# Kernel tuning notes

Hardware: AMD Instinct MI355X
Metric: run time of the kernel (lower is better)

The kernel has to match this reference:

```python
import jax, jax.numpy as jnp
import numpy as np

B, M, N_CTR, K = 16, 2048, 512, 32
DIM, DEPTH, HEADS = 384, 6, 6
EMB = 48  # fourier embedding dim (48//6 = 8 freqs per axis, basis [3,24])


def make_basis():
    e = (2.0 ** np.arange(EMB // 6)).astype(np.float32) * np.pi  # [8]
    z = np.zeros(EMB // 6, np.float32)
    basis = np.stack([np.concatenate([e, z, z]),
                      np.concatenate([z, e, z]),
                      np.concatenate([z, z, e])])  # [3, 24]
    return jnp.asarray(basis)


def fourier_embed(x, basis):
    # x [..., 3] -> [..., 48]  (sin/cos of 24 frequency projections)
    p = jnp.einsum('...d,de->...e', x, basis)
    return jnp.concatenate([jnp.sin(p), jnp.cos(p)], axis=-1)


def fps_idx(pos, n):
    # farthest point sampling, deterministic start at index 0. pos [M,3] -> [n]
    d0 = jnp.sum((pos - pos[0]) ** 2, -1)
    def step(d, _):
        i = jnp.argmax(d)
        d = jnp.minimum(d, jnp.sum((pos - pos[i]) ** 2, -1))
        return d, i
    _, idxs = jax.lax.scan(step, d0, None, length=n - 1)
    return jnp.concatenate([jnp.zeros(1, jnp.int32), idxs.astype(jnp.int32)])


def layernorm(x, g, b, eps=1e-6):
    m = jnp.mean(x, -1, keepdims=True)
    v = jnp.var(x, -1, keepdims=True)
    return (x - m) * jax.lax.rsqrt(v + eps) * g + b


def _lin(key, fi, fo):
    kw, kb = jax.random.split(key)
    w = jax.random.normal(kw, (fi, fo), jnp.float32) / np.sqrt(fi)
    b = jax.random.normal(kb, (fo,), jnp.float32) * 0.01
    return w, b


def setup_inputs() -> dict:
    key = jax.random.key(0)
    ks = jax.random.split(key, 16)
    pc = jax.random.uniform(ks[0], (B, M, 3), jnp.float32)
    embed_w, embed_b = _lin(ks[1], 3 + EMB, DIM)
    lw1, lb1 = _lin(ks[2], 3 + EMB, 256)
    lw2, lb2 = _lin(ks[3], 256, 256)
    gw1, gb1 = _lin(ks[4], 256, 256)
    gw2, gb2 = _lin(ks[5], 256, DIM)
    def stack_lin(k, fi, fo):
        kk = jax.random.split(k, DEPTH)
        ws, bs = zip(*[_lin(kk[i], fi, fo) for i in range(DEPTH)])
        return jnp.stack(ws), jnp.stack(bs)
    qkv_w, qkv_b = stack_lin(ks[6], DIM, 3 * DIM)
    proj_w, proj_b = stack_lin(ks[7], DIM, DIM)
    fc1_w, fc1_b = stack_lin(ks[8], DIM, 4 * DIM)
    fc2_w, fc2_b = stack_lin(ks[9], 4 * DIM, DIM)
    return dict(
        pc=pc, embed_w=embed_w, embed_b=embed_b,
        lw1=lw1, lb1=lb1, lw2=lw2, lb2=lb2,
        gw1=gw1, gb1=gb1, gw2=gw2, gb2=gb2,
        ln1_g=jnp.ones((DEPTH, DIM)), ln1_b=jnp.zeros((DEPTH, DIM)),
        qkv_w=qkv_w, qkv_b=qkv_b, proj_w=proj_w, proj_b=proj_b,
        gamma1=jax.random.normal(ks[10], (DEPTH, DIM)) * 0.1,
        ln2_g=jnp.ones((DEPTH, DIM)), ln2_b=jnp.zeros((DEPTH, DIM)),
        fc1_w=fc1_w, fc1_b=fc1_b, fc2_w=fc2_w, fc2_b=fc2_b,
        gamma2=jax.random.normal(ks[11], (DEPTH, DIM)) * 0.1,
        lnf_g=jnp.ones((DIM,)), lnf_b=jnp.zeros((DIM,)),
    )


def reference(pc, embed_w, embed_b, lw1, lb1, lw2, lb2, gw1, gb1, gw2, gb2,
              ln1_g, ln1_b, qkv_w, qkv_b, proj_w, proj_b, gamma1,
              ln2_g, ln2_b, fc1_w, fc1_b, fc2_w, fc2_b, gamma2, lnf_g, lnf_b):
    basis = make_basis()
    # --- FPS centers (per batch) ---
    idx = jax.vmap(lambda p: fps_idx(p, N_CTR))(pc)                 # [B,N]
    centers = jnp.take_along_axis(pc, idx[:, :, None], axis=1)      # [B,N,3]
    # --- KNN graph: for each center, K nearest of the M points ---
    d2 = jnp.sum((centers[:, :, None, :] - pc[:, None, :, :]) ** 2, -1)  # [B,N,M]
    _, nn_idx = jax.lax.top_k(-d2, K)                               # [B,N,K]
    # --- PointConv: gather -> local MLP -> max-scatter -> global MLP ---
    src = jax.vmap(lambda p, i: p[i])(pc, nn_idx)                   # [B,N,K,3]
    rel = src - centers[:, :, None, :]
    feat = jnp.concatenate([rel, fourier_embed(rel, basis)], -1)    # [B,N,K,51]
    h = jax.nn.relu(feat @ lw1 + lb1) @ lw2 + lb2                   # [B,N,K,256]
    h = jnp.max(h, axis=2)  # scatter_max over edges == max over K neighbors
    x = jax.nn.relu(h @ gw1 + gb1) @ gw2 + gb2                      # [B,N,DIM]
    # --- positional embedding tokens ---
    pe = jnp.concatenate([centers, fourier_embed(centers, basis)], -1) @ embed_w + embed_b
    x = x + pe
    # --- ViT blocks (pre-LN, LayerScale, eval mode: no dropout/droppath) ---
    hd = DIM // HEADS
    scale = hd ** -0.5
    for l in range(DEPTH):
        xn = layernorm(x, ln1_g[l], ln1_b[l])
        qkv = (xn @ qkv_w[l] + qkv_b[l]).reshape(B, N_CTR, 3, HEADS, hd)
        q, k, v = jnp.moveaxis(qkv, 2, 0)                           # [B,N,H,hd]
        att = jax.nn.softmax(jnp.einsum('bqhd,bkhd->bhqk', q, k) * scale, axis=-1)
        o = jnp.einsum('bhqk,bkhd->bqhd', att, v).reshape(B, N_CTR, DIM)
        x = x + gamma1[l] * (o @ proj_w[l] + proj_b[l])
        xn = layernorm(x, ln2_g[l], ln2_b[l])
        mlp = jax.nn.gelu(xn @ fc1_w[l] + fc1_b[l], approximate=False) @ fc2_w[l] + fc2_b[l]
        x = x + gamma2[l] * mlp
    out = layernorm(x, lnf_g, lnf_b)
    return out, centers
```

## Files before the change

kernel.cpp:

```cpp
#include <hip/hip_runtime.h>
#include <math.h>

#define NB 16
#define NM 2048
#define NCTR 512
#define NK 32
#define NDIM 384

typedef unsigned long long ull;
typedef unsigned int uint;
typedef unsigned short ushort;
typedef __attribute__((ext_vector_type(8))) short bf16x8;
typedef __attribute__((ext_vector_type(4))) float f32x4;

__device__ __forceinline__ float dist2_exact(float ax, float ay, float az,
                                             float bx, float by, float bz) {
  float dx = __fsub_rn(ax, bx);
  float dy = __fsub_rn(ay, by);
  float dz = __fsub_rn(az, bz);
  return __fadd_rn(__fadd_rn(__fmul_rn(dx, dx), __fmul_rn(dy, dy)),
                   __fmul_rn(dz, dz));
}

__device__ __forceinline__ float gelu_f(float x) {
  return 0.5f * x * (1.0f + erff(x * 0.70710678118654752f));
}

__device__ __forceinline__ ushort f2bf(float f) {
  uint u = __float_as_uint(f);
  return (ushort)((u + 0x7FFFu + ((u >> 16) & 1u)) >> 16);
}
__device__ __forceinline__ float bf2f(ushort h) {
  return __uint_as_float(((uint)h) << 16);
}

__device__ __forceinline__ void cvt8(float4 p, float4 q, uint4& hi, uint4& lo) {
  float v0 = p.x, v1 = p.y, v2 = p.z, v3 = p.w;
  float v4 = q.x, v5 = q.y, v6 = q.z, v7 = q.w;
  ushort h0 = f2bf(v0), h1 = f2bf(v1), h2 = f2bf(v2), h3 = f2bf(v3);
  ushort h4 = f2bf(v4), h5 = f2bf(v5), h6 = f2bf(v6), h7 = f2bf(v7);
  ushort l0 = f2bf(v0 - bf2f(h0)), l1 = f2bf(v1 - bf2f(h1));
  ushort l2 = f2bf(v2 - bf2f(h2)), l3 = f2bf(v3 - bf2f(h3));
  ushort l4 = f2bf(v4 - bf2f(h4)), l5 = f2bf(v5 - bf2f(h5));
  ushort l6 = f2bf(v6 - bf2f(h6)), l7 = f2bf(v7 - bf2f(h7));
  hi.x = (uint)h0 | ((uint)h1 << 16); hi.y = (uint)h2 | ((uint)h3 << 16);
  hi.z = (uint)h4 | ((uint)h5 << 16); hi.w = (uint)h6 | ((uint)h7 << 16);
  lo.x = (uint)l0 | ((uint)l1 << 16); lo.y = (uint)l2 | ((uint)l3 << 16);
  lo.z = (uint)l4 | ((uint)l5 << 16); lo.w = (uint)l6 | ((uint)l7 << 16);
}

__global__ __launch_bounds__(256)
void fps_kernel(const float* __restrict__ pc, float* __restrict__ centers) {
  int b = blockIdx.x;
  __shared__ float4 pos4[NM];
  __shared__ ull red[2][4];
  const float* pb = pc + (size_t)b * (NM * 3);
  int tid = threadIdx.x, lane = tid & 63, wv = tid >> 6;
  float px[8], py[8], pz[8];
#pragma unroll
  for (int i = 0; i < 8; ++i) {
    int p = tid + 256 * i;
    float x = pb[3 * p], y = pb[3 * p + 1], z = pb[3 * p + 2];
    px[i] = x; py[i] = y; pz[i] = z;
    pos4[p] = make_float4(x, y, z, 0.f);
  }
  __syncthreads();
  float* cb = centers + (size_t)b * (NCTR * 3);
  float4 s0 = pos4[0];
  float sx = s0.x, sy = s0.y, sz = s0.z;
  if (tid == 0) { cb[0] = sx; cb[1] = sy; cb[2] = sz; }
  float d[8];
  for (int n = 1; n < NCTR; ++n) {
    ull best = 0;
#pragma unroll
    for (int i = 0; i < 8; ++i) {
      int p = tid + 256 * i;
      float nd = dist2_exact(px[i], py[i], pz[i], sx, sy, sz);
      d[i] = (n == 1) ? nd : fminf(d[i], nd);
      ull key = ((ull)__float_as_uint(d[i]) << 32) | (unsigned)(0x7FFFFFFF - p);
      best = best > key ? best : key;
    }
#pragma unroll
    for (int off = 32; off; off >>= 1) {
      ull o = __shfl_xor(best, off);
      best = best > o ? best : o;
    }
    if (lane == 0) red[n & 1][wv] = best;
    __syncthreads();
    ull g0 = red[n & 1][0], g1 = red[n & 1][1];
    ull g2 = red[n & 1][2], g3 = red[n & 1][3];
    ull ga = g0 > g1 ? g0 : g1;
    ull gc2 = g2 > g3 ? g2 : g3;
    ull gb = ga > gc2 ? ga : gc2;
    int j = 0x7FFFFFFF - (int)(unsigned)(gb & 0xFFFFFFFFull);
    float4 np = pos4[j];
    sx = np.x; sy = np.y; sz = np.z;
    if (tid == 0) { cb[n * 3] = sx; cb[n * 3 + 1] = sy; cb[n * 3 + 2] = sz; }
  }
}

__global__ __launch_bounds__(256, 2)
void knn_kernel(const float* __restrict__ pc, const float* __restrict__ centers,
                int* __restrict__ nn) {
  __shared__ float pos[NM * 3];
  int b = blockIdx.x >> 7;
  int n0 = (blockIdx.x & 127) << 2;
  const float* pb = pc + (size_t)b * (NM * 3);
  for (int i = threadIdx.x; i < NM * 3; i += 256) pos[i] = pb[i];
  __syncthreads();
  int wv = threadIdx.x >> 6, lane = threadIdx.x & 63;
  int gc = b * NCTR + n0 + wv;
  float cx = centers[gc * 3], cy = centers[gc * 3 + 1], cz = centers[gc * 3 + 2];
  ull key[32];
  ull gmin[4];
#pragma unroll
  for (int g = 0; g < 4; ++g) {
    gmin[g] = ~0ull;
#pragma unroll
    for (int i = 0; i < 8; ++i) {
      int r = g * 8 + i;
      int p = lane + (r << 6);
      float nd = dist2_exact(pos[3 * p], pos[3 * p + 1], pos[3 * p + 2], cx, cy, cz);
      key[r] = ((ull)__float_as_uint(nd) << 11) | (unsigned)p;
      gmin[g] = gmin[g] < key[r] ? gmin[g] : key[r];
    }
  }
  ull a01 = gmin[0] < gmin[1] ? gmin[0] : gmin[1];
  ull a23 = gmin[2] < gmin[3] ? gmin[2] : gmin[3];
  ull lmin = a01 < a23 ? a01 : a23;
  int* nnc = nn + (size_t)gc * NK;
  for (int round = 0; round < NK; ++round) {
    ull w = lmin;
#pragma unroll
    for (int off = 32; off; off >>= 1) {
      ull o = __shfl_xor(w, off);
      w = w < o ? w : o;
    }
    if (lmin == w) {
      nnc[round] = (int)(w & 2047ull);
#pragma unroll
      for (int g = 0; g < 4; ++g) {
        if (gmin[g] == w) {
          gmin[g] = ~0ull;
#pragma unroll
          for (int i = 0; i < 8; ++i) {
            int r = g * 8 + i;
            key[r] = (key[r] == w) ? ~0ull : key[r];
            gmin[g] = gmin[g] < key[r] ? gmin[g] : key[r];
          }
        }
      }
      ull b01 = gmin[0] < gmin[1] ? gmin[0] : gmin[1];
      ull b23 = gmin[2] < gmin[3] ? gmin[2] : gmin[3];
      lmin = b01 < b23 ? b01 : b23;
    }
  }
}

__global__ __launch_bounds__(256)
void wconv(const float* __restrict__ W, ushort* __restrict__ out, int K8, int N,
           int Ksrc) {
  int c = blockIdx.x * 256 + threadIdx.x;
  if (c >= K8 * N) return;
  int kb = c / N, n = c - kb * N;
  float v[8];
#pragma unroll
  for (int i = 0; i < 8; ++i) {
    int row = kb * 8 + i;
    v[i] = (row < Ksrc) ? W[(size_t)row * N + n] : 0.f;
  }
  float4 p, q;
  p.x = v[0]; p.y = v[1]; p.z = v[2]; p.w = v[3];
  q.x = v[4]; q.y = v[5]; q.z = v[6]; q.w = v[7];
  uint4 hi, lo;
  cvt8(p, q, hi, lo);
  *(uint4*)(out + (size_t)c * 8) = hi;
  *(uint4*)(out + (size_t)(K8 * N + c) * 8) = lo;
}

__global__ __launch_bounds__(256, 2)
void edge_mfma(const float* __restrict__ pc, const float* __restrict__ centers,
               const int* __restrict__ nn, const ushort* __restrict__ lw1s,
               const float* __restrict__ lb1, const ushort* __restrict__ lw2s,
               const float* __restrict__ lb2, float* __restrict__ h) {
  __shared__ __align__(16) ushort featH[4096], featL[4096];
  __shared__ __align__(16) ushort t1H[16384], t1L[16384];
  int tid = threadIdx.x;
  int w = tid >> 6, lane = tid & 63;
  int l15 = lane & 15, l4 = lane >> 4;
  int wbase = w << 6;
  {
    int e = tid >> 2, s = tid & 3;
    int ge = blockIdx.x * 64 + e;
    int c = ge >> 5;
    int b = c >> 9;
    int j = nn[ge];
    const float* sp = pc + ((size_t)b * NM + j) * 3;
    float rx = sp[0] - centers[c * 3];
    float ry = sp[1] - centers[c * 3 + 1];
    float rz = sp[2] - centers[c * 3 + 2];
    auto putk = [&](int k, float v) {
      ushort hi = f2bf(v);
      ushort lo = f2bf(v - bf2f(hi));
      int idx = ((k >> 3) * 64 + e) * 8 + (k & 7);
      featH[idx] = hi;
      featL[idx] = lo;
    };
    if (s < 3) {
      float r = (s == 0) ? rx : (s == 1) ? ry : rz;
#pragma unroll
      for (int f = 0; f < 8; ++f) {
        float ef = (float)(M_PI * (double)(1 << f));
        float p = r * ef;
        putk(3 + 8 * s + f, sinf(p));
        putk(27 + 8 * s + f, cosf(p));
      }
    } else {
      putk(0, rx);
      putk(1, ry);
      putk(2, rz);
#pragma unroll
      for (int k = 51; k < 64; ++k) putk(k, 0.f);
    }
  }
  __syncthreads();
  const ushort* lw1H = lw1s;
  const ushort* lw1L = lw1s + 8 * 256 * 8;
  f32x4 acc1[4][4];
#pragma unroll
  for (int i = 0; i < 4; ++i)
#pragma unroll
    for (int j = 0; j < 4; ++j) acc1[i][j] = (f32x4){0.f, 0.f, 0.f, 0.f};
#pragma unroll
  for (int ks = 0; ks < 2; ++ks) {
    bf16x8 ah[4], al[4];
#pragma unroll
    for (int fm = 0; fm < 4; ++fm) {
      int idx = ((ks * 4 + l4) * 64 + fm * 16 + l15) * 8;
      ah[fm] = *(const bf16x8*)&featH[idx];
      al[fm] = *(const bf16x8*)&featL[idx];
    }
#pragma unroll
    for (int fn = 0; fn < 4; ++fn) {
      int col = wbase + fn * 16 + l15;
      size_t boff = ((size_t)(ks * 4 + l4) * 256 + col) * 8;
      bf16x8 bh = *(const bf16x8*)(lw1H + boff);
      bf16x8 bl = *(const bf16x8*)(lw1L + boff);
#pragma unroll
      for (int fm = 0; fm < 4; ++fm) {
        acc1[fm][fn] = __builtin_amdgcn_mfma_f32_16x16x32_bf16(al[fm], bh, acc1[fm][fn], 0, 0, 0);
        acc1[fm][fn] = __builtin_amdgcn_mfma_f32_16x16x32_bf16(ah[fm], bl, acc1[fm][fn], 0, 0, 0);
        acc1[fm][fn] = __builtin_amdgcn_mfma_f32_16x16x32_bf16(ah[fm], bh, acc1[fm][fn], 0, 0, 0);
      }
    }
  }
#pragma unroll
  for (int fn = 0; fn < 4; ++fn) {
    int chan = wbase + fn * 16 + l15;
    float bias = lb1[chan];
    int kb = chan >> 3, k7 = chan & 7;
#pragma unroll
    for (int fm = 0; fm < 4; ++fm) {
#pragma unroll
      for (int r = 0; r < 4; ++r) {
        int edge = fm * 16 + l4 * 4 + r;
        float v = fmaxf(acc1[fm][fn][r] + bias, 0.f);
        ushort hi = f2bf(v);
        ushort lo = f2bf(v - bf2f(hi));
        int idx = (kb * 64 + edge) * 8 + k7;
        t1H[idx] = hi;
        t1L[idx] = lo;
      }
    }
  }
  __syncthreads();
  const ushort* lw2H = lw2s;
  const ushort* lw2L = lw2s + 32 * 256 * 8;
  f32x4 acc2[4][4];
#pragma unroll
  for (int i = 0; i < 4; ++i)
#pragma unroll
    for (int j = 0; j < 4; ++j) acc2[i][j] = (f32x4){0.f, 0.f, 0.f, 0.f};
#pragma unroll
  for (int ks = 0; ks < 8; ++ks) {
    bf16x8 ah[4], al[4];
#pragma unroll
    for (int fm = 0; fm < 4; ++fm) {
      int idx = ((ks * 4 + l4) * 64 + fm * 16 + l15) * 8;
      ah[fm] = *(const bf16x8*)&t1H[idx];
      al[fm] = *(const bf16x8*)&t1L[idx];
    }
#pragma unroll
    for (int fn = 0; fn < 4; ++fn) {
      int col = wbase + fn * 16 + l15;
      size_t boff = ((size_t)(ks * 4 + l4) * 256 + col) * 8;
      bf16x8 bh = *(const bf16x8*)(lw2H + boff);
      bf16x8 bl = *(const bf16x8*)(lw2L + boff);
#pragma unroll
      for (int fm = 0; fm < 4; ++fm) {
        acc2[fm][fn] = __builtin_amdgcn_mfma_f32_16x16x32_bf16(al[fm], bh, acc2[fm][fn], 0, 0, 0);
        acc2[fm][fn] = __builtin_amdgcn_mfma_f32_16x16x32_bf16(ah[fm], bl, acc2[fm][fn], 0, 0, 0);
        acc2[fm][fn] = __builtin_amdgcn_mfma_f32_16x16x32_bf16(ah[fm], bh, acc2[fm][fn], 0, 0, 0);
      }
    }
  }
#pragma unroll
  for (int fn = 0; fn < 4; ++fn) {
    int col = wbase + fn * 16 + l15;
    float m0 = -INFINITY, m1 = -INFINITY;
#pragma unroll
    for (int r = 0; r < 4; ++r) {
      m0 = fmaxf(m0, fmaxf(acc2[0][fn][r], acc2[1][fn][r]));
      m1 = fmaxf(m1, fmaxf(acc2[2][fn][r], acc2[3][fn][r]));
    }
    m0 = fmaxf(m0, __shfl_xor(m0, 16));
    m0 = fmaxf(m0, __shfl_xor(m0, 32));
    m1 = fmaxf(m1, __shfl_xor(m1, 16));
    m1 = fmaxf(m1, __shfl_xor(m1, 32));
    if (l4 == 0) {
      float bias = lb2[col];
      int c0 = blockIdx.x * 2;
      h[(size_t)c0 * 256 + col] = m0 + bias;
      h[(size_t)(c0 + 1) * 256 + col] = m1 + bias;
    }
  }
}

template <int EPI>
__global__ __launch_bounds__(256, 2)
void gemm_x3(const float* __restrict__ A, const ushort* __restrict__ Wh,
             const ushort* __restrict__ Wl, const float* __restrict__ bias,
             const float* __restrict__ gamma, const float* __restrict__ resid,
             float* __restrict__ C, int M, int N, int K) {
  __shared__ __align__(16) ushort Ah[4096], Al[4096], Bh[4096], Bl[4096];
  int tid = threadIdx.x;
  int bn = blockIdx.x << 7, bm = blockIdx.y << 7;
  int wid = tid >> 6, lane = tid & 63;
  int wr = wid >> 1, wc = wid & 1;
  int l15 = lane & 15, l4 = lane >> 4;

  int arow = tid >> 1, akb0 = (tid & 1) << 1;
  const float* Ap = A + (size_t)(bm + arow) * K + (akb0 << 3);
  int wkb = tid >> 7, wn = tid & 127;

  f32x4 acc[4][4];
#pragma unroll
  for (int i = 0; i < 4; ++i)
#pragma unroll
    for (int j = 0; j < 4; ++j) acc[i][j] = (f32x4){0.f, 0.f, 0.f, 0.f};

  float4 a0 = *(const float4*)(Ap + 0);
  float4 a1 = *(const float4*)(Ap + 4);
  float4 a2 = *(const float4*)(Ap + 8);
  float4 a3 = *(const float4*)(Ap + 12);
  size_t wo1 = ((size_t)wkb * N + bn + wn) * 8;
  size_t wo2 = ((size_t)(wkb + 2) * N + bn + wn) * 8;
  uint4 w0 = *(const uint4*)(Wh + wo1);
  uint4 w1 = *(const uint4*)(Wh + wo2);
  uint4 w2 = *(const uint4*)(Wl + wo1);
  uint4 w3 = *(const uint4*)(Wl + wo2);

  int nkt = K >> 5;
  for (int kt = 0; kt < nkt; ++kt) {
    uint4 h0, l0, h1, l1;
    cvt8(a0, a1, h0, l0);
    cvt8(a2, a3, h1, l1);
    *(uint4*)&Ah[(akb0 * 128 + arow) * 8] = h0;
    *(uint4*)&Ah[((akb0 + 1) * 128 + arow) * 8] = h1;
    *(uint4*)&Al[(akb0 * 128 + arow) * 8] = l0;
    *(uint4*)&Al[((akb0 + 1) * 128 + arow) * 8] = l1;
    *(uint4*)&Bh[tid * 8] = w0;
    *(uint4*)&Bh[(tid + 256) * 8] = w1;
    *(uint4*)&Bl[tid * 8] = w2;
    *(uint4*)&Bl[(tid + 256) * 8] = w3;
    __syncthreads();
    if (kt + 1 < nkt) {
      const float* Apn = Ap + ((kt + 1) << 5);
      a0 = *(const float4*)(Apn + 0);
      a1 = *(const float4*)(Apn + 4);
      a2 = *(const float4*)(Apn + 8);
      a3 = *(const float4*)(Apn + 12);
      size_t b1 = ((size_t)((kt + 1) * 4 + wkb) * N + bn + wn) * 8;
      size_t b2 = ((size_t)((kt + 1) * 4 + wkb + 2) * N + bn + wn) * 8;
      w0 = *(const uint4*)(Wh + b1);
      w1 = *(const uint4*)(Wh + b2);
      w2 = *(const uint4*)(Wl + b1);
      w3 = *(const uint4*)(Wl + b2);
    }
    bf16x8 ahf[4], alf[4];
#pragma unroll
    for (int fm = 0; fm < 4; ++fm) {
      int ci = l4 * 128 + wr * 64 + fm * 16 + l15;
      ahf[fm] = *(bf16x8*)&Ah[ci * 8];
      alf[fm] = *(bf16x8*)&Al[ci * 8];
    }
#pragma unroll
    for (int fn = 0; fn < 4; ++fn) {
      int ci = l4 * 128 + wc * 64 + fn * 16 + l15;
      bf16x8 bh = *(bf16x8*)&Bh[ci * 8];
      bf16x8 bl = *(bf16x8*)&Bl[ci * 8];
#pragma unroll
      for (int fm = 0; fm < 4; ++fm) {
        acc[fm][fn] = __builtin_amdgcn_mfma_f32_16x16x32_bf16(alf[fm], bh, acc[fm][fn], 0, 0, 0);
        acc[fm][fn] = __builtin_amdgcn_mfma_f32_16x16x32_bf16(ahf[fm], bl, acc[fm][fn], 0, 0, 0);
        acc[fm][fn] = __builtin_amdgcn_mfma_f32_16x16x32_bf16(ahf[fm], bh, acc[fm][fn], 0, 0, 0);
      }
    }
    __syncthreads();
  }

#pragma unroll
  for (int fn = 0; fn < 4; ++fn) {
    int col = bn + wc * 64 + fn * 16 + l15;
    float bv = bias[col];
    float gv = (EPI == 3) ? gamma[col] : 0.f;
#pragma unroll
    for (int fm = 0; fm < 4; ++fm) {
      int row0 = bm + wr * 64 + fm * 16 + l4 * 4;
#pragma unroll
      for (int r = 0; r < 4; ++r) {
        float v = acc[fm][fn][r] + bv;
        if (EPI == 1) v = fmaxf(v, 0.f);
        else if (EPI == 2) v = gelu_f(v);
        else if (EPI == 3) v = resid[(size_t)(row0 + r) * N + col] + gv * v;
        C[(size_t)(row0 + r) * N + col] = v;
      }
    }
  }
}

__global__ __launch_bounds__(256)
void pe_add(const float* __restrict__ centers, const float* __restrict__ ew,
            const float* __restrict__ eb, float* x) {
  __shared__ float fc[51];
  int c = blockIdx.x, tid = threadIdx.x;
  if (tid < 24) {
    int a = tid >> 3, f = tid & 7;
    float coord = centers[c * 3 + a];
    float p = coord * (float)(M_PI * (double)(1 << f));
    fc[3 + tid] = sinf(p);
    fc[27 + tid] = cosf(p);
  } else if (tid < 27) {
    fc[tid - 24] = centers[c * 3 + (tid - 24)];
  }
  __syncthreads();
  for (int j = tid; j < NDIM; j += 256) {
    float acc = eb[j];
#pragma unroll
    for (int d = 0; d < 51; ++d) acc = fmaf(fc[d], ew[d * NDIM + j], acc);
    x[(size_t)c * NDIM + j] += acc;
  }
}

__global__ __launch_bounds__(256)
void ln_f32(const float* __restrict__ x, const float* __restrict__ g,
            const float* __restrict__ b, float* __restrict__ y) {
  int row = (blockIdx.x << 2) + (threadIdx.x >> 6);
  int lane = threadIdx.x & 63;
  const float* xr = x + (size_t)row * NDIM;
  float v[6];
#pragma unroll
  for (int i = 0; i < 6; ++i) v[i] = xr[lane + (i << 6)];
  float s = 0.f;
#pragma unroll
  for (int i = 0; i < 6; ++i) s += v[i];
#pragma unroll
  for (int off = 32; off; off >>= 1) s += __shfl_xor(s, off);
  float m = s / 384.f;
  float var = 0.f;
#pragma unroll
  for (int i = 0; i < 6; ++i) { float dd = v[i] - m; var += dd * dd; }
#pragma unroll
  for (int off = 32; off; off >>= 1) var += __shfl_xor(var, off);
  var = var / 384.f;
  float rs = 1.f / sqrtf(var + 1e-6f);
#pragma unroll
  for (int i = 0; i < 6; ++i) {
    int cc = lane + (i << 6);
    y[(size_t)row * NDIM + cc] = (v[i] - m) * rs * g[cc] + b[cc];
  }
}

__global__ __launch_bounds__(256, 2)
void attn_mfma(const float* __restrict__ qkv, float* __restrict__ o) {
  __shared__ __align__(16) ushort kTH[4096], kTL[4096];
  __shared__ __align__(16) ushort vSH[4096], vSL[4096];
  __shared__ __align__(16) ushort pSH[8192], pSL[8192];
  int bi = blockIdx.x;
  int qt = bi & 3;
  int hh = (bi >> 2) % 6;
  int b = bi / 24;
  int tid = threadIdx.x;
  int w = tid >> 6, lane = tid & 63;
  int l15 = lane & 15, l4 = lane >> 4;
  const float* base = qkv + (size_t)(b * NCTR) * 1152;
  int qbase = qt * 128 + w * 32;

  bf16x8 qh[2][2], ql[2][2];
#pragma unroll
  for (int qr = 0; qr < 2; ++qr) {
#pragma unroll
    for (int ds = 0; ds < 2; ++ds) {
      const float* qp = base + (size_t)(qbase + qr * 16 + l15) * 1152 + hh * 64 +
                        ds * 32 + l4 * 8;
      float4 f0 = *(const float4*)qp;
      float4 f1 = *(const float4*)(qp + 4);
      uint4 hi, lo;
      cvt8(f0, f1, hi, lo);
      qh[qr][ds] = *(bf16x8*)&hi;
      ql[qr][ds] = *(bf16x8*)&lo;
    }
  }

  f32x4 oacc[2][4];
#pragma unroll
  for (int i = 0; i < 2; ++i)
#pragma unroll
    for (int j = 0; j < 4; ++j) oacc[i][j] = (f32x4){0.f, 0.f, 0.f, 0.f};
  float m_[2][4], l_[2][4];
#pragma unroll
  for (int i = 0; i < 2; ++i)
#pragma unroll
    for (int r = 0; r < 4; ++r) { m_[i][r] = -INFINITY; l_[i][r] = 0.f; }

  ushort* pHw = pSH + w * 2048;
  ushort* pLw = pSL + w * 2048;

  for (int ch = 0; ch < 8; ++ch) {
    {
      int key = tid & 63, dgh = tid >> 6;
      const float* kp = base + (size_t)(ch * 64 + key) * 1152 + 384 + hh * 64;
#pragma unroll
      for (int i = 0; i < 2; ++i) {
        int dg = dgh * 2 + i;
        float4 f0 = *(const float4*)(kp + dg * 8);
        float4 f1 = *(const float4*)(kp + dg * 8 + 4);
        uint4 hi, lo;
        cvt8(f0, f1, hi, lo);
        *(uint4*)&kTH[(dg * 64 + key) * 8] = hi;
        *(uint4*)&kTL[(dg * 64 + key) * 8] = lo;
      }
      int d = tid & 63, kb2 = tid >> 6;
#pragma unroll
      for (int i = 0; i < 2; ++i) {
        int kb = kb2 + i * 4;
        float vv[8];
#pragma unroll
        for (int j = 0; j < 8; ++j)
          vv[j] = base[(size_t)(ch * 64 + kb * 8 + j) * 1152 + 768 + hh * 64 + d];
        float4 f0, f1;
        f0.x = vv[0]; f0.y = vv[1]; f0.z = vv[2]; f0.w = vv[3];
        f1.x = vv[4]; f1.y = vv[5]; f1.z = vv[6]; f1.w = vv[7];
        uint4 hi, lo;
        cvt8(f0, f1, hi, lo);
        *(uint4*)&vSH[(kb * 64 + d) * 8] = hi;
        *(uint4*)&vSL[(kb * 64 + d) * 8] = lo;
      }
    }
    __syncthreads();

    f32x4 sacc[2][4];
#pragma unroll
    for (int i = 0; i < 2; ++i)
#pragma unroll
      for (int j = 0; j < 4; ++j) sacc[i][j] = (f32x4){0.f, 0.f, 0.f, 0.f};
#pragma unroll
    for (int ds = 0; ds < 2; ++ds) {
#pragma unroll
      for (int kc = 0; kc < 4; ++kc) {
        int idx = ((ds * 4 + l4) * 64 + kc * 16 + l15) * 8;
        bf16x8 bh = *(const bf16x8*)&kTH[idx];
        bf16x8 bl = *(const bf16x8*)&kTL[idx];
#pragma unroll
        for (int qr = 0; qr < 2; ++qr) {
          sacc[qr][kc] = __builtin_amdgcn_mfma_f32_16x16x32_bf16(ql[qr][ds], bh, sacc[qr][kc], 0, 0, 0);
          sacc[qr][kc] = __builtin_amdgcn_mfma_f32_16x16x32_bf16(qh[qr][ds], bl, sacc[qr][kc], 0, 0, 0);
          sacc[qr][kc] = __builtin_amdgcn_mfma_f32_16x16x32_bf16(qh[qr][ds], bh, sacc[qr][kc], 0, 0, 0);
        }
      }
    }

    float t[2][4];
#pragma unroll
    for (int qr = 0; qr < 2; ++qr)
#pragma unroll
      for (int r = 0; r < 4; ++r) {
        float a0 = sacc[qr][0][r] * 0.125f; sacc[qr][0][r] = a0;
        float a1 = sacc[qr][1][r] * 0.125f; sacc[qr][1][r] = a1;
        float a2 = sacc[qr][2][r] * 0.125f; sacc[qr][2][r] = a2;
        float a3 = sacc[qr][3][r] * 0.125f; sacc[qr][3][r] = a3;
        t[qr][r] = fmaxf(fmaxf(a0, a1), fmaxf(a2, a3));
      }
#pragma unroll
    for (int off = 1; off < 16; off <<= 1)
#pragma unroll
      for (int qr = 0; qr < 2; ++qr)
#pragma unroll
        for (int r = 0; r < 4; ++r)
          t[qr][r] = fmaxf(t[qr][r], __shfl_xor(t[qr][r], off));
    float f_[2][4];
#pragma unroll
    for (int qr = 0; qr < 2; ++qr)
#pragma unroll
      for (int r = 0; r < 4; ++r) {
        float mn = fmaxf(m_[qr][r], t[qr][r]);
        f_[qr][r] = expf(m_[qr][r] - mn);
        m_[qr][r] = mn;
      }
#pragma unroll
    for (int qr = 0; qr < 2; ++qr)
#pragma unroll
      for (int dc = 0; dc < 4; ++dc)
#pragma unroll
        for (int r = 0; r < 4; ++r) oacc[qr][dc][r] *= f_[qr][r];
    float sm[2][4];
#pragma unroll
    for (int qr = 0; qr < 2; ++qr)
#pragma unroll
      for (int r = 0; r < 4; ++r) {
        float p0 = expf(sacc[qr][0][r] - m_[qr][r]); sacc[qr][0][r] = p0;
        float p1 = expf(sacc[qr][1][r] - m_[qr][r]); sacc[qr][1][r] = p1;
        float p2 = expf(sacc[qr][2][r] - m_[qr][r]); sacc[qr][2][r] = p2;
        float p3 = expf(sacc[qr][3][r] - m_[qr][r]); sacc[qr][3][r] = p3;
        sm[qr][r] = ((p0 + p1) + (p2 + p3));
      }
#pragma unroll
    for (int off = 1; off < 16; off <<= 1)
#pragma unroll
      for (int qr = 0; qr < 2; ++qr)
#pragma unroll
        for (int r = 0; r < 4; ++r)
          sm[qr][r] += __shfl_xor(sm[qr][r], off);
#pragma unroll
    for (int qr = 0; qr < 2; ++qr)
#pragma unroll
      for (int r = 0; r < 4; ++r) l_[qr][r] = l_[qr][r] * f_[qr][r] + sm[qr][r];

#pragma unroll
    for (int qr = 0; qr < 2; ++qr)
#pragma unroll
      for (int kc = 0; kc < 4; ++kc)
#pragma unroll
        for (int r = 0; r < 4; ++r) {
          float pv = sacc[qr][kc][r];
          ushort hi = f2bf(pv);
          ushort lo = f2bf(pv - bf2f(hi));
          int k = kc * 16 + l15;
          int qrow = qr * 16 + l4 * 4 + r;
          int idx = ((k >> 3) * 32 + qrow) * 8 + (k & 7);
          pHw[idx] = hi;
          pLw[idx] = lo;
        }

#pragma unroll
    for (int ks = 0; ks < 2; ++ks) {
      bf16x8 pah[2], pal[2];
#pragma unroll
      for (int qr = 0; qr < 2; ++qr) {
        int idx = ((ks * 4 + l4) * 32 + qr * 16 + l15) * 8;
        pah[qr] = *(const bf16x8*)&pHw[idx];
        pal[qr] = *(const bf16x8*)&pLw[idx];
      }
#pragma unroll
      for (int dc = 0; dc < 4; ++dc) {
        int idx = ((ks * 4 + l4) * 64 + dc * 16 + l15) * 8;
        bf16x8 vh = *(const bf16x8*)&vSH[idx];
        bf16x8 vl = *(const bf16x8*)&vSL[idx];
#pragma unroll
        for (int qr = 0; qr < 2; ++qr) {
          oacc[qr][dc] = __builtin_amdgcn_mfma_f32_16x16x32_bf16(pal[qr], vh, oacc[qr][dc], 0, 0, 0);
          oacc[qr][dc] = __builtin_amdgcn_mfma_f32_16x16x32_bf16(pah[qr], vl, oacc[qr][dc], 0, 0, 0);
          oacc[qr][dc] = __builtin_amdgcn_mfma_f32_16x16x32_bf16(pah[qr], vh, oacc[qr][dc], 0, 0, 0);
        }
      }
    }
    __syncthreads();
  }

  float il[2][4];
#pragma unroll
  for (int qr = 0; qr < 2; ++qr)
#pragma unroll
    for (int r = 0; r < 4; ++r) il[qr][r] = 1.f / l_[qr][r];
#pragma unroll
  for (int qr = 0; qr < 2; ++qr)
#pragma unroll
    for (int dc = 0; dc < 4; ++dc)
#pragma unroll
      for (int r = 0; r < 4; ++r) {
        int row = b * NCTR + qbase + qr * 16 + l4 * 4 + r;
        int col = hh * 64 + dc * 16 + l15;
        o[(size_t)row * NDIM + col] = oacc[qr][dc][r] * il[qr][r];
      }
}

extern "C" void kernel_launch(void* const* d_in, const int* in_sizes, int n_in,
                              void* d_out, int out_size, void* d_ws, size_t ws_size,
                              hipStream_t stream) {
  const float* pc      = (const float*)d_in[0];
  const float* embed_w = (const float*)d_in[1];
  const float* embed_b = (const float*)d_in[2];
  const float* lw1     = (const float*)d_in[3];
  const float* lb1     = (const float*)d_in[4];
  const float* lw2     = (const float*)d_in[5];
  const float* lb2     = (const float*)d_in[6];
  const float* gw1     = (const float*)d_in[7];
  const float* gb1     = (const float*)d_in[8];
  const float* gw2     = (const float*)d_in[9];
  const float* gb2     = (const float*)d_in[10];
  const float* ln1_g   = (const float*)d_in[11];
  const float* ln1_b   = (const float*)d_in[12];
  const float* qkv_w   = (const float*)d_in[13];
  const float* qkv_b   = (const float*)d_in[14];
  const float* proj_w  = (const float*)d_in[15];
  const float* proj_b  = (const float*)d_in[16];
  const float* gamma1  = (const float*)d_in[17];
  const float* ln2_g   = (const float*)d_in[18];
  const float* ln2_b   = (const float*)d_in[19];
  const float* fc1_w   = (const float*)d_in[20];
  const float* fc1_b   = (const float*)d_in[21];
  const float* fc2_w   = (const float*)d_in[22];
  const float* fc2_b   = (const float*)d_in[23];
  const float* gamma2  = (const float*)d_in[24];
  const float* lnf_g   = (const float*)d_in[25];
  const float* lnf_b   = (const float*)d_in[26];

  float* out = (float*)d_out;
  float* centers = out + (size_t)NB * NCTR * NDIM;

  int* nn = (int*)d_ws;
  float* fws = (float*)d_ws;
  float* h  = fws + 262144;
  float* x  = h + 8192 * 256;
  float* xn = x + 8192 * 384;
  float* F  = xn + 8192 * 384;
  ushort* wsplit = (ushort*)(fws + 21233664);

  size_t wofs = 0;
  ushort* qkvH[6]; ushort* projH[6]; ushort* fc1H[6]; ushort* fc2H[6];
  auto convp = [&](const float* w, int Kpad, int N, int Ksrc) -> ushort* {
    ushort* dst = wsplit + wofs;
    int K8 = Kpad >> 3, total = K8 * N;
    wconv<<<(total + 255) / 256, 256, 0, stream>>>(w, dst, K8, N, Ksrc);
    wofs += (size_t)2 * Kpad * N;
    return dst;
  };
  for (int l = 0; l < 6; ++l) qkvH[l] = convp(qkv_w + (size_t)l * 384 * 1152, 384, 1152, 384);
  for (int l = 0; l < 6; ++l) projH[l] = convp(proj_w + (size_t)l * 384 * 384, 384, 384, 384);
  for (int l = 0; l < 6; ++l) fc1H[l] = convp(fc1_w + (size_t)l * 384 * 1536, 384, 1536, 384);
  for (int l = 0; l < 6; ++l) fc2H[l] = convp(fc2_w + (size_t)l * 1536 * 384, 1536, 384, 1536);
  ushort* g1H = convp(gw1, 256, 256, 256);
  ushort* g2H = convp(gw2, 256, 384, 256);
  ushort* lw1s = convp(lw1, 64, 256, 51);
  ushort* lw2s = convp(lw2, 256, 256, 256);

  fps_kernel<<<NB, 256, 0, stream>>>(pc, centers);
  knn_kernel<<<2048, 256, 0, stream>>>(pc, centers, nn);
  edge_mfma<<<4096, 256, 0, stream>>>(pc, centers, nn, lw1s, lb1, lw2s, lb2, h);

  gemm_x3<1><<<dim3(2, 64), 256, 0, stream>>>(h, g1H, g1H + 256 * 256, gb1,
                                              nullptr, nullptr, xn, 8192, 256, 256);
  gemm_x3<0><<<dim3(3, 64), 256, 0, stream>>>(xn, g2H, g2H + 256 * 384, gb2,
                                              nullptr, nullptr, x, 8192, 384, 256);
  pe_add<<<8192, 256, 0, stream>>>(centers, embed_w, embed_b, x);

  for (int l = 0; l < 6; ++l) {
    ln_f32<<<2048, 256, 0, stream>>>(x, ln1_g + l * 384, ln1_b + l * 384, xn);
    gemm_x3<0><<<dim3(9, 64), 256, 0, stream>>>(
        xn, qkvH[l], qkvH[l] + 384 * 1152, qkv_b + l * 1152, nullptr, nullptr, F,
        8192, 1152, 384);
    attn_mfma<<<384, 256, 0, stream>>>(F, xn);
    gemm_x3<3><<<dim3(3, 64), 256, 0, stream>>>(
        xn, projH[l], projH[l] + 384 * 384, proj_b + l * 384, gamma1 + l * 384, x, x,
        8192, 384, 384);
    ln_f32<<<2048, 256, 0, stream>>>(x, ln2_g + l * 384, ln2_b + l * 384, xn);
    gemm_x3<2><<<dim3(12, 64), 256, 0, stream>>>(
        xn, fc1H[l], fc1H[l] + 384 * 1536, fc1_b + l * 1536, nullptr, nullptr, F,
        8192, 1536, 384);
    gemm_x3<3><<<dim3(3, 64), 256, 0, stream>>>(
        F, fc2H[l], fc2H[l] + 1536 * 384, fc2_b + l * 384, gamma2 + l * 384, x, x,
        8192, 384, 1536);
  }
  ln_f32<<<2048, 256, 0, stream>>>(x, lnf_g, lnf_b, out);
}
```

Measured before the change: 2.073 ms.

## Store activations pre-split as bf16 hi/lo pairs to skip per-tile conversion

Producers (edge kernel, GEMM epilogues, layernorm, attention output) now write activations as bf16 hi/lo ushort pairs instead of fp32. GEMM and attention load these directly into LDS, which removes the repeated fp32-to-bf16x2 split on every tile load, and reuse across column blocks no longer repeats that work. Memory traffic stays about the same (two ushorts per float), but conversion ALU work is removed from the GEMM inner loop. Stacked per-layer weights are also converted in one launch per tensor rather than six. The workspace layout is reorganized to hold the split buffers.

```diff
diff --git a/kernel.cpp b/kernel.cpp
--- a/kernel.cpp
+++ b/kernel.cpp
@@ -47,6 +47,13 @@
   hi.z = (uint)h4 | ((uint)h5 << 16); hi.w = (uint)h6 | ((uint)h7 << 16);
   lo.x = (uint)l0 | ((uint)l1 << 16); lo.y = (uint)l2 | ((uint)l3 << 16);
   lo.z = (uint)l4 | ((uint)l5 << 16); lo.w = (uint)l6 | ((uint)l7 << 16);
+}
+
+__device__ __forceinline__ void split_store(float v, ushort* H, ushort* L,
+                                            size_t off) {
+  ushort hi = f2bf(v);
+  H[off] = hi;
+  L[off] = f2bf(v - bf2f(hi));
 }
 
 __global__ __launch_bounds__(256)
@@ -182,7 +189,8 @@
 void edge_mfma(const float* __restrict__ pc, const float* __restrict__ centers,
                const int* __restrict__ nn, const ushort* __restrict__ lw1s,
                const float* __restrict__ lb1, const ushort* __restrict__ lw2s,
-               const float* __restrict__ lb2, float* __restrict__ h) {
+               const float* __restrict__ lb2, ushort* __restrict__ hH,
+               ushort* __restrict__ hL) {
   __shared__ __align__(16) ushort featH[4096], featL[4096];
   __shared__ __align__(16) ushort t1H[16384], t1L[16384];
   int tid = threadIdx.x;
@@ -320,18 +328,20 @@
     if (l4 == 0) {
       float bias = lb2[col];
       int c0 = blockIdx.x * 2;
-      h[(size_t)c0 * 256 + col] = m0 + bias;
-      h[(size_t)(c0 + 1) * 256 + col] = m1 + bias;
-    }
-  }
-}
-
-template <int EPI>
+      split_store(m0 + bias, hH, hL, (size_t)c0 * 256 + col);
+      split_store(m1 + bias, hH, hL, (size_t)(c0 + 1) * 256 + col);
+    }
+  }
+}
+
+template <int EPI, int OUTS>
 __global__ __launch_bounds__(256, 2)
-void gemm_x3(const float* __restrict__ A, const ushort* __restrict__ Wh,
-             const ushort* __restrict__ Wl, const float* __restrict__ bias,
-             const float* __restrict__ gamma, const float* __restrict__ resid,
-             float* __restrict__ C, int M, int N, int K) {
+void gemm_s(const ushort* __restrict__ AH, const ushort* __restrict__ AL,
+            const ushort* __restrict__ Wh, const ushort* __restrict__ Wl,
+            const float* __restrict__ bias, const float* __restrict__ gamma,
+            const float* __restrict__ resid, float* __restrict__ C,
+            ushort* __restrict__ CH, ushort* __restrict__ CL,
+            int M, int N, int K) {
   __shared__ __align__(16) ushort Ah[4096], Al[4096], Bh[4096], Bl[4096];
   int tid = threadIdx.x;
   int bn = blockIdx.x << 7, bm = blockIdx.y << 7;
@@ -340,7 +350,8 @@
   int l15 = lane & 15, l4 = lane >> 4;
 
   int arow = tid >> 1, akb0 = (tid & 1) << 1;
-  const float* Ap = A + (size_t)(bm + arow) * K + (akb0 << 3);
+  const ushort* ApH = AH + (size_t)(bm + arow) * K + (akb0 << 3);
+  const ushort* ApL = AL + (size_t)(bm + arow) * K + (akb0 << 3);
   int wkb = tid >> 7, wn = tid & 127;
 
   f32x4 acc[4][4];
@@ -349,10 +360,10 @@
 #pragma unroll
     for (int j = 0; j < 4; ++j) acc[i][j] = (f32x4){0.f, 0.f, 0.f, 0.f};
 
-  float4 a0 = *(const float4*)(Ap + 0);
-  float4 a1 = *(const float4*)(Ap + 4);
-  float4 a2 = *(const float4*)(Ap + 8);
-  float4 a3 = *(const float4*)(Ap + 12);
+  uint4 a0 = *(const uint4*)(ApH + 0);
+  uint4 a1 = *(const uint4*)(ApH + 8);
+  uint4 a2 = *(const uint4*)(ApL + 0);
+  uint4 a3 = *(const uint4*)(ApL + 8);
   size_t wo1 = ((size_t)wkb * N + bn + wn) * 8;
   size_t wo2 = ((size_t)(wkb + 2) * N + bn + wn) * 8;
   uint4 w0 = *(const uint4*)(Wh + wo1);
@@ -362,24 +373,20 @@
 
   int nkt = K >> 5;
   for (int kt = 0; kt < nkt; ++kt) {
-    uint4 h0, l0, h1, l1;
-    cvt8(a0, a1, h0, l0);
-    cvt8(a2, a3, h1, l1);
-    *(uint4*)&Ah[(akb0 * 128 + arow) * 8] = h0;
-    *(uint4*)&Ah[((akb0 + 1) * 128 + arow) * 8] = h1;
-    *(uint4*)&Al[(akb0 * 128 + arow) * 8] = l0;
-    *(uint4*)&Al[((akb0 + 1) * 128 + arow) * 8] = l1;
+    *(uint4*)&Ah[(akb0 * 128 + arow) * 8] = a0;
+    *(uint4*)&Ah[((akb0 + 1) * 128 + arow) * 8] = a1;
+    *(uint4*)&Al[(akb0 * 128 + arow) * 8] = a2;
+    *(uint4*)&Al[((akb0 + 1) * 128 + arow) * 8] = a3;
     *(uint4*)&Bh[tid * 8] = w0;
     *(uint4*)&Bh[(tid + 256) * 8] = w1;
     *(uint4*)&Bl[tid * 8] = w2;
     *(uint4*)&Bl[(tid + 256) * 8] = w3;
     __syncthreads();
     if (kt + 1 < nkt) {
-      const float* Apn = Ap + ((kt + 1) << 5);
-      a0 = *(const float4*)(Apn + 0);
-      a1 = *(const float4*)(Apn + 4);
-      a2 = *(const float4*)(Apn + 8);
-      a3 = *(const float4*)(Apn + 12);
+      a0 = *(const uint4*)(ApH + (kt + 1) * 32 + 0);
+      a1 = *(const uint4*)(ApH + (kt + 1) * 32 + 8);
+      a2 = *(const uint4*)(ApL + (kt + 1) * 32 + 0);
+      a3 = *(const uint4*)(ApL + (kt + 1) * 32 + 8);
       size_t b1 = ((size_t)((kt + 1) * 4 + wkb) * N + bn + wn) * 8;
       size_t b2 = ((size_t)((kt + 1) * 4 + wkb + 2) * N + bn + wn) * 8;
       w0 = *(const uint4*)(Wh + b1);
@@ -423,7 +430,9 @@
         if (EPI == 1) v = fmaxf(v, 0.f);
         else if (EPI == 2) v = gelu_f(v);
         else if (EPI == 3) v = resid[(size_t)(row0 + r) * N + col] + gv * v;
-        C[(size_t)(row0 + r) * N + col] = v;
+        size_t off = (size_t)(row0 + r) * N + col;
+        if (OUTS == 0) C[off] = v;
+        else split_store(v, CH, CL, off);
       }
     }
   }
@@ -481,8 +490,40 @@
   }
 }
 
+__global__ __launch_bounds__(256)
+void ln_split(const float* __restrict__ x, const float* __restrict__ g,
+              const float* __restrict__ b, ushort* __restrict__ yH,
+              ushort* __restrict__ yL) {
+  int row = (blockIdx.x << 2) + (threadIdx.x >> 6);
+  int lane = threadIdx.x & 63;
+  const float* xr = x + (size_t)row * NDIM;
+  float v[6];
+#pragma unroll
+  for (int i = 0; i < 6; ++i) v[i] = xr[lane + (i << 6)];
+  float s = 0.f;
+#pragma unroll
+  for (int i = 0; i < 6; ++i) s += v[i];
+#pragma unroll
+  for (int off = 32; off; off >>= 1) s += __shfl_xor(s, off);
+  float m = s / 384.f;
+  float var = 0.f;
+#pragma unroll
+  for (int i = 0; i < 6; ++i) { float dd = v[i] - m; var += dd * dd; }
+#pragma unroll
+  for (int off = 32; off; off >>= 1) var += __shfl_xor(var, off);
+  var = var / 384.f;
+  float rs = 1.f / sqrtf(var + 1e-6f);
+#pragma unroll
+  for (int i = 0; i < 6; ++i) {
+    int cc = lane + (i << 6);
+    float yv = (v[i] - m) * rs * g[cc] + b[cc];
+    split_store(yv, yH, yL, (size_t)row * NDIM + cc);
+  }
+}
+
 __global__ __launch_bounds__(256, 2)
-void attn_mfma(const float* __restrict__ qkv, float* __restrict__ o) {
+void attn_mfma(const ushort* __restrict__ FH, const ushort* __restrict__ FL,
+               ushort* __restrict__ oH, ushort* __restrict__ oL) {
   __shared__ __align__(16) ushort kTH[4096], kTL[4096];
   __shared__ __align__(16) ushort vSH[4096], vSL[4096];
   __shared__ __align__(16) ushort pSH[8192], pSL[8192];
@@ -493,7 +534,8 @@
   int tid = threadIdx.x;
   int w = tid >> 6, lane = tid & 63;
   int l15 = lane & 15, l4 = lane >> 4;
-  const float* base = qkv + (size_t)(b * NCTR) * 1152;
+  const ushort* baseH = FH + (size_t)(b * NCTR) * 1152;
+  const ushort* baseL = FL + (size_t)(b * NCTR) * 1152;
   int qbase = qt * 128 + w * 32;
 
   bf16x8 qh[2][2], ql[2][2];
@@ -501,14 +543,9 @@
   for (int qr = 0; qr < 2; ++qr) {
 #pragma unroll
     for (int ds = 0; ds < 2; ++ds) {
-      const float* qp = base + (size_t)(qbase + qr * 16 + l15) * 1152 + hh * 64 +
-                        ds * 32 + l4 * 8;
-      float4 f0 = *(const float4*)qp;
-      float4 f1 = *(const float4*)(qp + 4);
-      uint4 hi, lo;
-      cvt8(f0, f1, hi, lo);
-      qh[qr][ds] = *(bf16x8*)&hi;
-      ql[qr][ds] = *(bf16x8*)&lo;
+      size_t off = (size_t)(qbase + qr * 16 + l15) * 1152 + hh * 64 + ds * 32 + l4 * 8;
+      qh[qr][ds] = *(const bf16x8*)(baseH + off);
+      ql[qr][ds] = *(const bf16x8*)(baseL + off);
     }
   }
 
@@ -529,32 +566,31 @@
   for (int ch = 0; ch < 8; ++ch) {
     {
       int key = tid & 63, dgh = tid >> 6;
-      const float* kp = base + (size_t)(ch * 64 + key) * 1152 + 384 + hh * 64;
+      size_t krow = (size_t)(ch * 64 + key) * 1152 + 384 + hh * 64;
 #pragma unroll
       for (int i = 0; i < 2; ++i) {
         int dg = dgh * 2 + i;
-        float4 f0 = *(const float4*)(kp + dg * 8);
-        float4 f1 = *(const float4*)(kp + dg * 8 + 4);
-        uint4 hi, lo;
-        cvt8(f0, f1, hi, lo);
-        *(uint4*)&kTH[(dg * 64 + key) * 8] = hi;
-        *(uint4*)&kTL[(dg * 64 + key) * 8] = lo;
+        *(uint4*)&kTH[(dg * 64 + key) * 8] = *(const uint4*)(baseH + krow + dg * 8);
+        *(uint4*)&kTL[(dg * 64 + key) * 8] = *(const uint4*)(baseL + krow + dg * 8);
       }
       int d = tid & 63, kb2 = tid >> 6;
 #pragma unroll
       for (int i = 0; i < 2; ++i) {
         int kb = kb2 + i * 4;
-        float vv[8];
-#pragma unroll
-        for (int j = 0; j < 8; ++j)
-          vv[j] = base[(size_t)(ch * 64 + kb * 8 + j) * 1152 + 768 + hh * 64 + d];
-        float4 f0, f1;
-        f0.x = vv[0]; f0.y = vv[1]; f0.z = vv[2]; f0.w = vv[3];
-        f1.x = vv[4]; f1.y = vv[5]; f1.z = vv[6]; f1.w = vv[7];
-        uint4 hi, lo;
-        cvt8(f0, f1, hi, lo);
-        *(uint4*)&vSH[(kb * 64 + d) * 8] = hi;
-        *(uint4*)&vSL[(kb * 64 + d) * 8] = lo;
+        ushort hv[8], lv[8];
+#pragma unroll
+        for (int j = 0; j < 8; ++j) {
+          size_t off = (size_t)(ch * 64 + kb * 8 + j) * 1152 + 768 + hh * 64 + d;
+          hv[j] = baseH[off];
+          lv[j] = baseL[off];
+        }
+        uint4 H, L;
+        H.x = (uint)hv[0] | ((uint)hv[1] << 16); H.y = (uint)hv[2] | ((uint)hv[3] << 16);
+        H.z = (uint)hv[4] | ((uint)hv[5] << 16); H.w = (uint)hv[6] | ((uint)hv[7] << 16);
+        L.x = (uint)lv[0] | ((uint)lv[1] << 16); L.y = (uint)lv[2] | ((uint)lv[3] << 16);
+        L.z = (uint)lv[4] | ((uint)lv[5] << 16); L.w = (uint)lv[6] | ((uint)lv[7] << 16);
+        *(uint4*)&vSH[(kb * 64 + d) * 8] = H;
+        *(uint4*)&vSL[(kb * 64 + d) * 8] = L;
       }
     }
     __syncthreads();
@@ -690,7 +726,7 @@
       for (int r = 0; r < 4; ++r) {
         int row = b * NCTR + qbase + qr * 16 + l4 * 4 + r;
         int col = hh * 64 + dc * 16 + l15;
-        o[(size_t)row * NDIM + col] = oacc[qr][dc][r] * il[qr][r];
+        split_store(oacc[qr][dc][r] * il[qr][r], oH, oL, (size_t)row * NDIM + col);
       }
 }
 
@@ -728,16 +764,18 @@
   float* out = (float*)d_out;
   float* centers = out + (size_t)NB * NCTR * NDIM;
 
-  int* nn = (int*)d_ws;
-  float* fws = (float*)d_ws;
-  float* h  = fws + 262144;
-  float* x  = h + 8192 * 256;
-  float* xn = x + 8192 * 384;
-  float* F  = xn + 8192 * 384;
-  ushort* wsplit = (ushort*)(fws + 21233664);
+  char* ws = (char*)d_ws;
+  int*    nn  = (int*)(ws + 0);
+  float*  x   = (float*)(ws + 1048576);
+  ushort* xnH = (ushort*)(ws + 13631488);
+  ushort* xnL = (ushort*)(ws + 19922944);
+  ushort* FH  = (ushort*)(ws + 26214400);
+  ushort* FL  = (ushort*)(ws + 51380224);
+  ushort* hH  = (ushort*)(ws + 76546048);
+  ushort* hL  = (ushort*)(ws + 80740352);
+  ushort* wsplit = (ushort*)(ws + 84934656);
 
   size_t wofs = 0;
-  ushort* qkvH[6]; ushort* projH[6]; ushort* fc1H[6]; ushort* fc2H[6];
   auto convp = [&](const float* w, int Kpad, int N, int Ksrc) -> ushort* {
     ushort* dst = wsplit + wofs;
     int K8 = Kpad >> 3, total = K8 * N;
@@ -745,41 +783,43 @@
     wofs += (size_t)2 * Kpad * N;
     return dst;
   };
-  for (int l = 0; l < 6; ++l) qkvH[l] = convp(qkv_w + (size_t)l * 384 * 1152, 384, 1152, 384);
-  for (int l = 0; l < 6; ++l) projH[l] = convp(proj_w + (size_t)l * 384 * 384, 384, 384, 384);
-  for (int l = 0; l < 6; ++l) fc1H[l] = convp(fc1_w + (size_t)l * 384 * 1536, 384, 1536, 384);
-  for (int l = 0; l < 6; ++l) fc2H[l] = convp(fc2_w + (size_t)l * 1536 * 384, 1536, 384, 1536);
-  ushort* g1H = convp(gw1, 256, 256, 256);
-  ushort* g2H = convp(gw2, 256, 384, 256);
+  ushort* qkvS = convp(qkv_w, 2304, 1152, 2304);
+  ushort* projS = convp(proj_w, 2304, 384, 2304);
+  ushort* fc1S = convp(fc1_w, 2304, 1536, 2304);
+  ushort* fc2S = convp(fc2_w, 9216, 384, 9216);
+  ushort* g1S  = convp(gw1, 256, 256, 256);
+  ushort* g2S  = convp(gw2, 256, 384, 256);
   ushort* lw1s = convp(lw1, 64, 256, 51);
   ushort* lw2s = convp(lw2, 256, 256, 256);
 
   fps_kernel<<<NB, 256, 0, stream>>>(pc, centers);
   knn_kernel<<<2048, 256, 0, stream>>>(pc, centers, nn);
-  edge_mfma<<<4096, 256, 0, stream>>>(pc, centers, nn, lw1s, lb1, lw2s, lb2, h);
-
-  gemm_x3<1><<<dim3(2, 64), 256, 0, stream>>>(h, g1H, g1H + 256 * 256, gb1,
-                                              nullptr, nullptr, xn, 8192, 256, 256);
-  gemm_x3<0><<<dim3(3, 64), 256, 0, stream>>>(xn, g2H, g2H + 256 * 384, gb2,
-                                              nullptr, nullptr, x, 8192, 384, 256);
+  edge_mfma<<<4096, 256, 0, stream>>>(pc, centers, nn, lw1s, lb1, lw2s, lb2, hH, hL);
+
+  gemm_s<1, 1><<<dim3(2, 64), 256, 0, stream>>>(hH, hL, g1S, g1S + 65536, gb1,
+                                                nullptr, nullptr, nullptr, xnH, xnL,
+                                                8192, 256, 256);
+  gemm_s<0, 0><<<dim3(3, 64), 256, 0, stream>>>(xnH, xnL, g2S, g2S + 98304, gb2,
+                                                nullptr, nullptr, x, nullptr, nullptr,
+                                                8192, 384, 256);
   pe_add<<<8192, 256, 0, stream>>>(centers, embed_w, embed_b, x);
 
   for (int l = 0; l < 6; ++l) {
-    ln_f32<<<2048, 256, 0, stream>>>(x, ln1_g + l * 384, ln1_b + l * 384, xn);
-    gemm_x3<0><<<dim3(9, 64), 256, 0, stream>>>(
-        xn, qkvH[l], qkvH[l] + 384 * 1152, qkv_b + l * 1152, nullptr, nullptr, F,
-        8192, 1152, 384);
-    attn_mfma<<<384, 256, 0, stream>>>(F, xn);
-    gemm_x3<3><<<dim3(3, 64), 256, 0, stream>>>(
-        xn, projH[l], projH[l] + 384 * 384, proj_b + l * 384, gamma1 + l * 384, x, x,
-        8192, 384, 384);
-    ln_f32<<<2048, 256, 0, stream>>>(x, ln2_g + l * 384, ln2_b + l * 384, xn);
-    gemm_x3<2><<<dim3(12, 64), 256, 0, stream>>>(
-        xn, fc1H[l], fc1H[l] + 384 * 1536, fc1_b + l * 1536, nullptr, nullptr, F,
-        8192, 1536, 384);
-    gemm_x3<3><<<dim3(3, 64), 256, 0, stream>>>(
-        F, fc2H[l], fc2H[l] + 1536 * 384, fc2_b + l * 384, gamma2 + l * 384, x, x,
-        8192, 384, 1536);
+    ln_split<<<2048, 256, 0, stream>>>(x, ln1_g + l * 384, ln1_b + l * 384, xnH, xnL);
+    gemm_s<0, 1><<<dim3(9, 64), 256, 0, stream>>>(
+        xnH, xnL, qkvS + (size_t)l * 442368, qkvS + 2654208 + (size_t)l * 442368,
+        qkv_b + l * 1152, nullptr, nullptr, nullptr, FH, FL, 8192, 1152, 384);
+    attn_mfma<<<384, 256, 0, stream>>>(FH, FL, xnH, xnL);
+    gemm_s<3, 0><<<dim3(3, 64), 256, 0, stream>>>(
+        xnH, xnL, projS + (size_t)l * 147456, projS + 884736 + (size_t)l * 147456,
+        proj_b + l * 384, gamma1 + l * 384, x, x, nullptr, nullptr, 8192, 384, 384);
+    ln_split<<<2048, 256, 0, stream>>>(x, ln2_g + l * 384, ln2_b + l * 384, xnH, xnL);
+    gemm_s<2, 1><<<dim3(12, 64), 256, 0, stream>>>(
+        xnH, xnL, fc1S + (size_t)l * 589824, fc1S + 3538944 + (size_t)l * 589824,
+        fc1_b + l * 1536, nullptr, nullptr, nullptr, FH, FL, 8192, 1536, 384);
+    gemm_s<3, 0><<<dim3(3, 64), 256, 0, stream>>>(
+        FH, FL, fc2S + (size_t)l * 589824, fc2S + 3538944 + (size_t)l * 589824,
+        fc2_b + l * 384, gamma2 + l * 384, x, x, nullptr, nullptr, 8192, 384, 1536);
   }
   ln_f32<<<2048, 256, 0, stream>>>(x, lnf_g, lnf_b, out);
 }
```

After: 2.026 ms. 1.02x faster.
